# Kernel optimization log

Hardware: AMD Instinct MI355X
Metric: run time of the kernel (lower is better)

The kernel has to match this reference:

```python
import jax, jax.numpy as jnp
import numpy as np

N_PTS = 500000
IN_DIM = 2
M_FOURIER = 32
J_WAVELET = 3
Q = 12
DEGREE = 3
N_CONTROL = 25
EMB_DIM = 2 * M_FOURIER + 2 * (2 ** J_WAVELET - 1)  # 78
LN_EPS = 1e-5


def make_open_uniform_knots(num_control, degree):
    n_knots = num_control + degree + 1  # 29
    if n_knots <= 2 * (degree + 1):
        return np.linspace(0.0, 1.0, n_knots).astype(np.float32)
    n_internal = n_knots - 2 * (degree + 1)
    internal = np.linspace(0.0, 1.0, n_internal + 2)[1:-1]
    return np.concatenate([np.zeros(degree + 1), internal, np.ones(degree + 1)]).astype(np.float32)

KNOTS = jnp.asarray(make_open_uniform_knots(N_CONTROL, DEGREE))


def bspline_basis(x, knots, degree, n_basis):
    # x: (M,) -> (M, n_basis); faithful (truncated) Cox-de-Boor as in source
    x = jnp.clip(x, knots[0], knots[-1])
    left = knots[:n_basis]
    right = knots[1:n_basis + 1]
    N = ((x[:, None] >= left) & (x[:, None] < right)).astype(x.dtype)
    last = ((x >= left[-1]) & (x <= right[-1])).astype(x.dtype)
    N = N.at[:, -1].set(last)
    for p in range(1, degree + 1):
        d1 = knots[p:p + n_basis] - knots[:n_basis]
        d2 = knots[p + 1:p + 1 + n_basis] - knots[1:1 + n_basis]
        c1 = jnp.where(d1 != 0, (x[:, None] - knots[:n_basis]) / jnp.where(d1 != 0, d1, 1.0), 0.0)
        c2 = jnp.where(d2 != 0, (knots[p + 1:p + 1 + n_basis] - x[:, None]) / jnp.where(d2 != 0, d2, 1.0), 0.0)
        N_shift = jnp.concatenate([N[:, 1:], jnp.zeros_like(N[:, :1])], axis=1)  # i+1 < n_basis guard
        N = c1 * N + c2 * N_shift
    return N


def wavelet_features_2d(z, J):
    x, t = z[:, 0], z[:, 1]
    feats = []
    for j in range(J):
        num_k = 2 ** j
        scale = max(0.5 / num_k, 0.001)
        centers = jnp.asarray([(k + 0.5) / num_k for k in range(num_k)], dtype=z.dtype)
        ux = x[:, None] - centers[None, :]
        ut = t[:, None] - centers[None, :]
        for u in (ux, ut):
            v = u / scale
            feats.append((1.0 - v * v) * jnp.exp(-0.5 * v * v))
    return jnp.concatenate(feats, axis=1)  # (N, 2*(2^J-1))


def setup_inputs() -> dict:
    key = jax.random.key(0)
    ks = jax.random.split(key, 6)
    xt = jax.random.uniform(ks[0], (N_PTS, IN_DIM), dtype=jnp.float32)
    B_fourier = jax.random.normal(ks[1], (M_FOURIER, IN_DIM), dtype=jnp.float32) * 1.0  # sigma_B
    ln_gamma = jnp.ones((EMB_DIM,), jnp.float32)
    ln_beta = jnp.zeros((EMB_DIM,), jnp.float32)
    W = jax.random.normal(ks[2], (Q, EMB_DIM), dtype=jnp.float32) * 0.05
    b_inner = jnp.zeros((Q,), jnp.float32)
    inner_scale = jnp.asarray(0.5, jnp.float32)
    coeffs = jax.random.normal(ks[3], (Q, N_CONTROL), dtype=jnp.float32) * 0.05
    a = jax.random.normal(ks[4], (Q, 1), dtype=jnp.float32) * 0.05
    b_out = jnp.zeros((1,), jnp.float32)
    return {"xt": xt, "B_fourier": B_fourier, "ln_gamma": ln_gamma, "ln_beta": ln_beta,
            "W": W, "b_inner": b_inner, "inner_scale": inner_scale, "coeffs": coeffs,
            "a": a, "b_out": b_out}


def reference(xt, B_fourier, ln_gamma, ln_beta, W, b_inner, inner_scale, coeffs, a, b_out):
    # Fourier features
    proj = (2.0 * np.pi) * (xt @ B_fourier.T)  # (N, M)
    scale = 1.0 / (np.sqrt(M_FOURIER) + 1e-12)
    F = jnp.concatenate([jnp.sin(proj) * scale, jnp.cos(proj) * scale], axis=1)
    # Wavelet features
    Wf = wavelet_features_2d(xt, J_WAVELET)
    emb = jnp.concatenate([F, Wf], axis=1)  # (N, 78)
    # LayerNorm
    mu = jnp.mean(emb, axis=-1, keepdims=True)
    var = jnp.mean(jnp.square(emb - mu), axis=-1, keepdims=True)
    emb = (emb - mu) / jnp.sqrt(var + LN_EPS) * ln_gamma + ln_beta
    # KAN B-spline core
    u_inner = emb @ W.T + b_inner  # (N, Q)
    s = 0.5 * (jnp.tanh(inner_scale * u_inner) + 1.0)
    B_flat = bspline_basis(s.reshape(-1), KNOTS, DEGREE, N_CONTROL)  # (N*Q, 25)
    B = B_flat.reshape(emb.shape[0], Q, N_CONTROL)
    phi = jnp.einsum('nqc,qc->nq', B, coeffs)
    u_out = phi @ a + b_out  # (N, 1)
    return u_out
```

## Files before the change

kernel.cpp:

```cpp
#include <hip/hip_runtime.h>
#include <hip/hip_bf16.h>
#include <math.h>

#define MF 32
#define EMB 78
#define NQ 12
#define NC 25
#define NSPAN 22
#define BLK 256
#define FSCALE 0.17677669529663688f

typedef __attribute__((ext_vector_type(8))) short short8;
typedef __attribute__((ext_vector_type(4))) float f32x4;

#define WS_A    0
#define WS_SGSB 768
#define WS_P    800

__device__ __forceinline__ float fast_rcp(float x) { return __builtin_amdgcn_rcpf(x); }
__device__ __forceinline__ float satf(float x) { return fminf(fmaxf(x, 0.0f), 1.0f); }

__device__ __forceinline__ unsigned pack2(float a, float b) {
    __hip_bfloat16 ha = __float2bfloat16(a), hb = __float2bfloat16(b);
    unsigned short ua, ub;
    __builtin_memcpy(&ua, &ha, 2); __builtin_memcpy(&ub, &hb, 2);
    return (unsigned)ua | ((unsigned)ub << 16);
}

__device__ __forceinline__ float4 deboor4(float s, int ii) {
    const float c22 = 1.0f / 22.0f;
    float k_m2 = satf((float)(ii - 2) * c22);
    float k_m1 = satf((float)(ii - 1) * c22);
    float k_0  = satf((float)(ii)     * c22);
    float k_p1 = satf((float)(ii + 1) * c22);
    float k_p2 = satf((float)(ii + 2) * c22);
    float k_p3 = satf((float)(ii + 3) * c22);
    float l1 = s - k_0, l2 = s - k_m1, l3 = s - k_m2;
    float r1 = k_p1 - s, r2 = k_p2 - s, r3 = k_p3 - s;
    float t0 = fast_rcp(r1 + l1);
    float N0 = r1 * t0, N1 = l1 * t0;
    float ta = N0 * fast_rcp(r1 + l2);
    float tb = N1 * fast_rcp(r2 + l1);
    N0 = r1 * ta;
    N1 = fmaf(l2, ta, r2 * tb);
    float N2 = l1 * tb;
    float tc = N0 * fast_rcp(r1 + l3);
    float td = N1 * fast_rcp(r2 + l2);
    float te = N2 * fast_rcp(r3 + l1);
    N0 = r1 * tc;
    N1 = fmaf(l3, tc, r2 * td);
    N2 = fmaf(l2, td, r3 * te);
    float N3 = l1 * te;
    return make_float4(N0, N1, N2, N3);
}

__device__ __forceinline__ float wgf(const float* g, const float* W, int q, int k) {
    if (q >= NQ || k >= EMB) return 0.0f;
    float v = g[k] * W[q * EMB + k];
    return (k < 2 * MF) ? v * FSCALE : v;
}

__global__ __launch_bounds__(256) void pikan_setup(
    const float* __restrict__ g, const float* __restrict__ be,
    const float* __restrict__ W, const float* __restrict__ bi,
    const float* __restrict__ coeffs, const float* __restrict__ a,
    float* __restrict__ ws)
{
    const int tid = threadIdx.x;
    unsigned* wsu = (unsigned*)ws;

    for (int i = tid; i < 768; i += 256) {
        int d = i & 3, l = (i >> 2) & 63, kt = i >> 8;
        int q = l & 15;
        int kb = kt * 32 + (l >> 4) * 8 + d * 2;
        wsu[WS_A + i] = pack2(wgf(g, W, q, kb), wgf(g, W, q, kb + 1));
    }
    if (tid < 16) {
        float sg = 0.f, sb = 0.f;
        if (tid < NQ) {
            for (int e = 0; e < EMB; ++e) {
                float w = W[tid * EMB + e];
                sg += g[e] * w;
                sb += be[e] * w;
            }
            sb += bi[tid];
        }
        ws[WS_SGSB + 2 * tid]     = sg;
        ws[WS_SGSB + 2 * tid + 1] = sb;
    }
    for (int i = tid; i < 16 * NSPAN; i += 256) {
        int q = i / NSPAN, ii = i - q * NSPAN;
        float4 o = make_float4(0.f, 0.f, 0.f, 0.f);
        if (q < NQ) {
            float f[4];
            #pragma unroll
            for (int j = 0; j < 4; ++j) {
                float u = (float)j / 3.0f;
                float s = ((float)ii + u) * (1.0f / 22.0f);
                float4 N = deboor4(s, ii);
                const float* cq = coeffs + q * NC + ii;
                f[j] = N.x * cq[0] + N.y * cq[1] + N.z * cq[2] + N.w * cq[3];
            }
            float c0 = f[0];
            float c1 = -5.5f * f[0] +  9.0f * f[1] -  4.5f * f[2] +  1.0f * f[3];
            float c2 =  9.0f * f[0] - 22.5f * f[1] + 18.0f * f[2] -  4.5f * f[3];
            float c3 = -4.5f * f[0] + 13.5f * f[1] - 13.5f * f[2] +  4.5f * f[3];
            float aq = a[q];
            o = make_float4(c0 * aq, c1 * aq, c2 * aq, c3 * aq);
        }
        reinterpret_cast<float4*>(ws + WS_P)[i] = o;
    }
}

__global__ __launch_bounds__(BLK, 4) void pikan_main(
    const float* __restrict__ xt, const float* __restrict__ Bf,
    const float* __restrict__ isc_p, const float* __restrict__ bout_p,
    const float* __restrict__ ws, float* __restrict__ out, int npts)
{
    __shared__ uint4  sEmb[4][256];
    __shared__ float4 sPoly[4][16 * NSPAN + 1];

    const int tid = threadIdx.x;
    for (int i = tid; i < 16 * NSPAN; i += BLK) {
        float4 v = reinterpret_cast<const float4*>(ws + WS_P)[i];
        sPoly[0][i] = v; sPoly[1][i] = v; sPoly[2][i] = v; sPoly[3][i] = v;
    }
    __syncthreads();

    const int l = tid & 63, w = tid >> 6;
    const int g16 = l >> 4, c16 = l & 15;
    const int sw = (l >> 1) & 3;
    uint4* myEmb = sEmb[w];
    const float4* myPoly = sPoly[l & 3];

    const uint4 af0 = reinterpret_cast<const uint4*>(ws)[0 * 64 + l];
    const uint4 af1 = reinterpret_cast<const uint4*>(ws)[1 * 64 + l];
    const uint4 af2 = reinterpret_cast<const uint4*>(ws)[2 * 64 + l];

    float sgq[4], sbq[4];
    #pragma unroll
    for (int r = 0; r < 4; ++r) {
        int q = g16 * 4 + r;
        sgq[r] = ws[WS_SGSB + 2 * q];
        sbq[r] = ws[WS_SGSB + 2 * q + 1];
    }

    const float kexp = -2.0f * isc_p[0] * 1.4426950408889634f;
    const float bout = bout_p[0];
    const int base = (blockIdx.x * 4 + w) * 128;

    const int pt0 = base + l, pt1 = base + 64 + l;
    float2 p0 = make_float2(0.f, 0.f), p1 = make_float2(0.f, 0.f);
    if (pt0 < npts) p0 = reinterpret_cast<const float2*>(xt)[pt0];
    if (pt1 < npts) p1 = reinterpret_cast<const float2*>(xt)[pt1];

    #pragma unroll 1
    for (int pass = 0; pass < 2; ++pass) {
        const int pt = pass ? pt1 : pt0;
        const bool valid = pt < npts;
        const float x = pass ? p1.x : p0.x;
        const float t = pass ? p1.y : p0.y;

        f32x4 acc[4];
        #pragma unroll
        for (int n = 0; n < 4; ++n) acc[n] = (f32x4){0.f, 0.f, 0.f, 0.f};

        auto stage = [&](uint4 a0, uint4 a1, uint4 a2, uint4 a3) {
            myEmb[l * 4 + (0 ^ sw)] = a0;
            myEmb[l * 4 + (1 ^ sw)] = a1;
            myEmb[l * 4 + (2 ^ sw)] = a2;
            myEmb[l * 4 + (3 ^ sw)] = a3;
        };
        auto mfma_kt = [&](uint4 au) {
            short8 af = __builtin_bit_cast(short8, au);
            #pragma unroll
            for (int n = 0; n < 4; ++n) {
                int p = n * 16 + c16;
                uint4 bu = myEmb[p * 4 + (g16 ^ sw)];
                short8 bf = __builtin_bit_cast(short8, bu);
                acc[n] = __builtin_amdgcn_mfma_f32_16x16x32_bf16(af, bf, acc[n], 0, 0, 0);
            }
        };

        float sumf = 0.f;
        unsigned spk[16], cpk[16];
        #pragma unroll
        for (int mp = 0; mp < 16; ++mp) {
            float rev0 = fmaf(x, Bf[4 * mp + 0], t * Bf[4 * mp + 1]);
            float rev1 = fmaf(x, Bf[4 * mp + 2], t * Bf[4 * mp + 3]);
#if __has_builtin(__builtin_amdgcn_fractf)
            float f0 = __builtin_amdgcn_fractf(rev0);
            float f1 = __builtin_amdgcn_fractf(rev1);
#else
            float f0 = rev0 - floorf(rev0);
            float f1 = rev1 - floorf(rev1);
#endif
            float s0 = __builtin_amdgcn_sinf(f0), s1 = __builtin_amdgcn_sinf(f1);
            float c0 = __builtin_amdgcn_cosf(f0), c1 = __builtin_amdgcn_cosf(f1);
            sumf += (s0 + s1) + (c0 + c1);
            spk[mp] = pack2(s0, s1);
            cpk[mp] = pack2(c0, c1);
        }
        stage(make_uint4(spk[0], spk[1], spk[2],  spk[3]),
              make_uint4(spk[4], spk[5], spk[6],  spk[7]),
              make_uint4(spk[8], spk[9], spk[10], spk[11]),
              make_uint4(spk[12], spk[13], spk[14], spk[15]));
        mfma_kt(af0);
        stage(make_uint4(cpk[0], cpk[1], cpk[2],  cpk[3]),
              make_uint4(cpk[4], cpk[5], cpk[6],  cpk[7]),
              make_uint4(cpk[8], cpk[9], cpk[10], cpk[11]),
              make_uint4(cpk[12], cpk[13], cpk[14], cpk[15]));
        mfma_kt(af1);

        float w14[14];
        float sumw = 0.f, ssw = 0.f;
        {
            int o = 0;
            #pragma unroll
            for (int j = 0; j < 3; ++j) {
                const int nk = 1 << j;
                const float inv = (float)(2 * nk);
                #pragma unroll
                for (int k = 0; k < nk; ++k) {
                    float c = ((float)k + 0.5f) / (float)nk;
                    float v = (x - c) * inv, v2 = v * v;
                    float f = (1.0f - v2) * __expf(-0.5f * v2);
                    w14[o + k] = f; sumw += f; ssw = fmaf(f, f, ssw);
                }
                #pragma unroll
                for (int k = 0; k < nk; ++k) {
                    float c = ((float)k + 0.5f) / (float)nk;
                    float v = (t - c) * inv, v2 = v * v;
                    float f = (1.0f - v2) * __expf(-0.5f * v2);
                    w14[o + nk + k] = f; sumw += f; ssw = fmaf(f, f, ssw);
                }
                o += 2 * nk;
            }
        }
        stage(make_uint4(pack2(w14[0], w14[1]), pack2(w14[2], w14[3]),
                         pack2(w14[4], w14[5]), pack2(w14[6], w14[7])),
              make_uint4(pack2(w14[8], w14[9]), pack2(w14[10], w14[11]),
                         pack2(w14[12], w14[13]), 0u),
              make_uint4(0u, 0u, 0u, 0u),
              make_uint4(0u, 0u, 0u, 0u));
        mfma_kt(af2);

        const float sum = fmaf(FSCALE, sumf, sumw);
        const float ssq = fmaf(FSCALE * FSCALE, 32.0f, ssw);
        const float mu = sum * (1.0f / EMB);
        float var = fmaf(-mu, mu, ssq * (1.0f / EMB));
        var = fmaxf(var, 0.0f);
        const float istd = rsqrtf(var + 1e-5f);

        float yout = 0.f;
        #pragma unroll
        for (int n = 0; n < 4; ++n) {
            float mun  = __shfl(mu,   n * 16 + c16);
            float istn = __shfl(istd, n * 16 + c16);
            float yn = 0.f;
            #pragma unroll
            for (int r = 0; r < 4; ++r) {
                float uq = fmaf(istn, fmaf(-mun, sgq[r], acc[n][r]), sbq[r]);
                float e2 = __builtin_amdgcn_exp2f(kexp * uq);
                float s = fast_rcp(1.0f + e2);
                float v = s * 22.0f;
                int ii = (int)v; ii = ii > 21 ? 21 : ii;
                float uu = v - (float)ii;
                float4 cc = myPoly[(g16 * 4 + r) * NSPAN + ii];
                yn += fmaf(fmaf(fmaf(cc.w, uu, cc.z), uu, cc.y), uu, cc.x);
            }
            yn += __shfl_xor(yn, 16);
            yn += __shfl_xor(yn, 32);
            if (g16 == n) yout = yn;
        }
        if (valid) out[pt] = yout + bout;
    }
}

extern "C" void kernel_launch(void* const* d_in, const int* in_sizes, int n_in,
                              void* d_out, int out_size, void* d_ws, size_t ws_size,
                              hipStream_t stream) {
    const float* xt          = (const float*)d_in[0];
    const float* Bf          = (const float*)d_in[1];
    const float* gamma       = (const float*)d_in[2];
    const float* beta        = (const float*)d_in[3];
    const float* W           = (const float*)d_in[4];
    const float* b_inner     = (const float*)d_in[5];
    const float* inner_scale = (const float*)d_in[6];
    const float* coeffs      = (const float*)d_in[7];
    const float* a           = (const float*)d_in[8];
    const float* b_out       = (const float*)d_in[9];
    float* out = (float*)d_out;
    float* ws  = (float*)d_ws;

    const int npts = in_sizes[0] / 2;
    pikan_setup<<<1, 256, 0, stream>>>(gamma, beta, W, b_inner, coeffs, a, ws);
    const int grid = (npts + 511) / 512;
    pikan_main<<<grid, BLK, 0, stream>>>(xt, Bf, inner_scale, b_out, ws, out, npts);
}
```

Baseline: 26.90 us.

## Unroll two-pass loop into interleaved phases and use bit-trick bf16 packing

The two point passes, previously serialized in an `unroll 1` loop, become two calls of a lambda. All feature and MFMA work for both points is issued before a batched set of shuffles and then both epilogues. The aim is to give the scheduler independent instruction streams to overlap transcendental, LDS and MFMA latencies. The bf16 conversion is also replaced by a manual round-to-nearest-even bit manipulation, which drops NaN handling and needs fewer instructions. Keeping both accumulator sets live raises register pressure and may lower occupancy.

```diff
diff --git a/kernel.cpp b/kernel.cpp
--- a/kernel.cpp
+++ b/kernel.cpp
@@ -25,6 +25,14 @@
     unsigned short ua, ub;
     __builtin_memcpy(&ua, &ha, 2); __builtin_memcpy(&ub, &hb, 2);
     return (unsigned)ua | ((unsigned)ub << 16);
+}
+
+__device__ __forceinline__ unsigned bfpair(float a, float b) {
+    unsigned ua = __builtin_bit_cast(unsigned, a);
+    unsigned ub = __builtin_bit_cast(unsigned, b);
+    ua += 0x7fffu + ((ua >> 16) & 1u);
+    ub += 0x7fffu + ((ub >> 16) & 1u);
+    return (ua >> 16) | (ub & 0xffff0000u);
 }
 
 __device__ __forceinline__ float4 deboor4(float s, int ii) {
@@ -154,14 +162,7 @@
     if (pt0 < npts) p0 = reinterpret_cast<const float2*>(xt)[pt0];
     if (pt1 < npts) p1 = reinterpret_cast<const float2*>(xt)[pt1];
 
-    #pragma unroll 1
-    for (int pass = 0; pass < 2; ++pass) {
-        const int pt = pass ? pt1 : pt0;
-        const bool valid = pt < npts;
-        const float x = pass ? p1.x : p0.x;
-        const float t = pass ? p1.y : p0.y;
-
-        f32x4 acc[4];
+    auto do_pass = [&](float x, float t, f32x4 (&acc)[4]) -> float2 {
         #pragma unroll
         for (int n = 0; n < 4; ++n) acc[n] = (f32x4){0.f, 0.f, 0.f, 0.f};
 
@@ -198,8 +199,8 @@
             float s0 = __builtin_amdgcn_sinf(f0), s1 = __builtin_amdgcn_sinf(f1);
             float c0 = __builtin_amdgcn_cosf(f0), c1 = __builtin_amdgcn_cosf(f1);
             sumf += (s0 + s1) + (c0 + c1);
-            spk[mp] = pack2(s0, s1);
-            cpk[mp] = pack2(c0, c1);
+            spk[mp] = bfpair(s0, s1);
+            cpk[mp] = bfpair(c0, c1);
         }
         stage(make_uint4(spk[0], spk[1], spk[2],  spk[3]),
               make_uint4(spk[4], spk[5], spk[6],  spk[7]),
@@ -237,10 +238,10 @@
                 o += 2 * nk;
             }
         }
-        stage(make_uint4(pack2(w14[0], w14[1]), pack2(w14[2], w14[3]),
-                         pack2(w14[4], w14[5]), pack2(w14[6], w14[7])),
-              make_uint4(pack2(w14[8], w14[9]), pack2(w14[10], w14[11]),
-                         pack2(w14[12], w14[13]), 0u),
+        stage(make_uint4(bfpair(w14[0], w14[1]), bfpair(w14[2], w14[3]),
+                         bfpair(w14[4], w14[5]), bfpair(w14[6], w14[7])),
+              make_uint4(bfpair(w14[8], w14[9]), bfpair(w14[10], w14[11]),
+                         bfpair(w14[12], w14[13]), 0u),
               make_uint4(0u, 0u, 0u, 0u),
               make_uint4(0u, 0u, 0u, 0u));
         mfma_kt(af2);
@@ -251,16 +252,31 @@
         float var = fmaf(-mu, mu, ssq * (1.0f / EMB));
         var = fmaxf(var, 0.0f);
         const float istd = rsqrtf(var + 1e-5f);
-
+        return make_float2(mu, istd);
+    };
+
+    f32x4 acc0[4], acc1[4];
+    float2 st0 = do_pass(p0.x, p0.y, acc0);
+    float2 st1 = do_pass(p1.x, p1.y, acc1);
+
+    float mun0[4], isn0[4], mun1[4], isn1[4];
+    #pragma unroll
+    for (int n = 0; n < 4; ++n) {
+        mun0[n] = __shfl(st0.x, n * 16 + c16);
+        isn0[n] = __shfl(st0.y, n * 16 + c16);
+        mun1[n] = __shfl(st1.x, n * 16 + c16);
+        isn1[n] = __shfl(st1.y, n * 16 + c16);
+    }
+
+    auto epi = [&](const f32x4 (&acc)[4], const float (&mun)[4],
+                   const float (&isn)[4]) -> float {
         float yout = 0.f;
         #pragma unroll
         for (int n = 0; n < 4; ++n) {
-            float mun  = __shfl(mu,   n * 16 + c16);
-            float istn = __shfl(istd, n * 16 + c16);
             float yn = 0.f;
             #pragma unroll
             for (int r = 0; r < 4; ++r) {
-                float uq = fmaf(istn, fmaf(-mun, sgq[r], acc[n][r]), sbq[r]);
+                float uq = fmaf(isn[n], fmaf(-mun[n], sgq[r], acc[n][r]), sbq[r]);
                 float e2 = __builtin_amdgcn_exp2f(kexp * uq);
                 float s = fast_rcp(1.0f + e2);
                 float v = s * 22.0f;
@@ -273,8 +289,13 @@
             yn += __shfl_xor(yn, 32);
             if (g16 == n) yout = yn;
         }
-        if (valid) out[pt] = yout + bout;
-    }
+        return yout;
+    };
+
+    float y0 = epi(acc0, mun0, isn0);
+    float y1 = epi(acc1, mun1, isn1);
+    if (pt0 < npts) out[pt0] = y0 + bout;
+    if (pt1 < npts) out[pt1] = y1 + bout;
 }
 
 extern "C" void kernel_launch(void* const* d_in, const int* in_sizes, int n_in,
```

Measured after the change: 31.56 us. 17.3% more time.
